# Performance work log

Measured on AMD Instinct MI355X. Metric: run time of the kernel, lower is better.

Reference implementation:

```python
import jax, jax.numpy as jnp
import numpy as np

# CycleFC1w1a constants (from init_kwargs / gen_offset)
IN_CH = 384
KH, KW = 1, 7  # cycle kernel; actual conv weight is 1x1
START = (KH * KW) // 2  # 3


def _gen_offset_x(C):
    # kernel_size[0] == 1 branch: off_y = 0, off_x[i] = (i + START) % KW - KW // 2
    i = jnp.arange(C)
    return (i + START) % KW - KW // 2  # int32, values in [-3, 3]


def setup_inputs() -> dict:
    key = jax.random.key(0)
    k1, k2, k3 = jax.random.split(key, 3)
    x = jax.random.normal(k1, (64, IN_CH, 32, 32), dtype=jnp.float32)
    weight = jax.random.normal(k2, (IN_CH, IN_CH), dtype=jnp.float32) * 0.05  # [out_ch, in_ch]
    bias = jax.random.normal(k3, (IN_CH,), dtype=jnp.float32) * 0.01
    return {"x": x, "weight": weight, "bias": bias}


def reference(x, weight, bias):
    B, C, H, W = x.shape
    # BinaryQuantizer forward: sign()
    xb = jnp.sign(x)
    wb = jnp.sign(weight)  # [O, C]

    # Fixed per-channel integer horizontal offsets -> exact shifted gather
    off_x = _gen_offset_x(C)                                  # [C]
    cols = jnp.arange(W)[None, :] + off_x[:, None]            # [C, W] sample col = w + off
    valid = (cols >= 0) & (cols < W)                          # zero-pad out of bounds
    cols_c = jnp.clip(cols, 0, W - 1)
    # gather along width per channel: [B, C, H, W]
    g = jnp.take_along_axis(xb, cols_c[None, :, None, :], axis=3)
    g = g * valid[None, :, None, :].astype(x.dtype)

    # pointwise (1x1) channel-mixing conv
    out = jnp.einsum('bchw,oc->bohw', g, wb) + bias[None, :, None, None]
    return out
```

## Files before the change

### kernel.cpp

```cpp
#include <hip/hip_runtime.h>
#include <stdint.h>


#define IN_CH 384
#define HH 32
#define WW 32
#define BB 64

constexpr uint64_t P7(int t) {
  uint64_t m = 0;
  for (int k = 0; k < 64; ++k)
    if (k % 7 == t) m |= (1ull << k);
  return m;
}
__device__ __constant__ uint64_t Pm[7] = {P7(0), P7(1), P7(2), P7(3), P7(4), P7(5), P7(6)};

__global__ __launch_bounds__(64) void cyc_prep(const float* __restrict__ wgt,
                                               const float* __restrict__ bias,
                                               uint64_t* __restrict__ wbg,
                                               float* __restrict__ bias2w) {
  const int o = blockIdx.x;
  const int lane = threadIdx.x;
  __shared__ uint64_t wb_sh[6];
#pragma unroll
  for (int j = 0; j < 6; ++j) {
    uint64_t m = __ballot(wgt[o * IN_CH + j * 64 + lane] < 0.0f);
    if (lane == 0) wb_sh[j] = m;
  }
  __syncthreads();
  if (lane < 6) wbg[o * 6 + lane] = wb_sh[lane];
  if (lane < WW) {
    const int w = lane;
    int nv = 0, corr = 0;
#pragma unroll
    for (int j = 0; j < 6; ++j) {
      uint64_t V = 0;
#pragma unroll
      for (int d = -3; d <= 3; ++d) {
        int wd = w + d;
        if (wd >= 0 && wd < WW) V |= Pm[(d - j + 14) % 7];
      }
      nv += __popcll(V);
      corr += __popcll(wb_sh[j] & ~V);
    }
    bias2w[o * WW + w] = bias[o] + (float)nv + 2.0f * (float)corr;
  }
}

__global__ __launch_bounds__(768) void cyc_pack(const float* __restrict__ x,
                                                uint32_t* __restrict__ G32) {
  const int t = threadIdx.x;
  const int lane = t & 63, wave = t >> 6;
  const int b = blockIdx.x >> 3;
  const int h0 = (blockIdx.x & 7) * 4;
  const int wcol = lane & 31, hhalf = lane >> 5;
#pragma unroll
  for (int p = 0; p < 2; ++p) {
    const int tau = wave + p * 12;
    const int r = tau / 6, j = tau % 6;
    const int c = j * 64 + lane;
    const int off = ((c % 7 + 3) % 7) - 3;
    const uint32_t shr = (off > 0) ? (uint32_t)off : 0u;
    const uint32_t shl = (off < 0) ? (uint32_t)(-off) : 0u;
    const float4* xp = reinterpret_cast<const float4*>(
        x + (size_t)((b * IN_CH + c) * HH + h0 + r) * WW);
    uint32_t myw = 0;
#pragma unroll
    for (int i = 0; i < 8; ++i) {
      float4 v = xp[i];
      myw |= (v.x < 0.0f ? 1u : 0u) << (i * 4 + 0);
      myw |= (v.y < 0.0f ? 1u : 0u) << (i * 4 + 1);
      myw |= (v.z < 0.0f ? 1u : 0u) << (i * 4 + 2);
      myw |= (v.w < 0.0f ? 1u : 0u) << (i * 4 + 3);
    }
    uint32_t s = (myw >> shr) << shl;
    constexpr uint32_t Mt[5] = {0xFFFF0000u, 0xFF00FF00u, 0xF0F0F0F0u,
                                0xCCCCCCCCu, 0xAAAAAAAAu};
#pragma unroll
    for (int stp = 0; stp < 5; ++stp) {
      const int js = 16 >> stp;
      const uint32_t M = Mt[stp];
      uint32_t y = __shfl_xor(s, js);
      s = (lane & js) ? ((s & M) | ((y >> js) & ~M))
                      : ((s & ~M) | ((y << js) & M));
    }
    G32[(((size_t)b * 6 + j) * 1024 + (h0 + r) * 32 + wcol) * 2 + hhalf] = s;
  }
}

__global__ __launch_bounds__(512) void cyc_gemm(const uint64_t* __restrict__ G,
                                                const uint64_t* __restrict__ wbg,
                                                const float* __restrict__ bias2w,
                                                float* __restrict__ out) {
  const int t = threadIdx.x;
  const int lane = t & 63, wave = t >> 6;
  const int b = blockIdx.x >> 3;
  const int oc = blockIdx.x & 7;
  const int o0 = oc * 48 + __builtin_amdgcn_readfirstlane(wave) * 6;

  uint64_t Wg[6][6];
  {
    const uint64_t* wp = wbg + (size_t)o0 * 6;
#pragma unroll
    for (int oo = 0; oo < 6; ++oo)
#pragma unroll
      for (int j = 0; j < 6; ++j) Wg[oo][j] = wp[oo * 6 + j];
  }
  const int w4 = (4 * lane) & 31;
  float4 bs[6];
#pragma unroll
  for (int oo = 0; oo < 6; ++oo)
    bs[oo] = *reinterpret_cast<const float4*>(bias2w + (o0 + oo) * WW + w4);

  const uint64_t* gb = G + (size_t)b * 6 * 1024;
  float* ob = out + ((size_t)b * IN_CH + o0) * (HH * WW);

#pragma unroll
  for (int pass = 0; pass < 4; ++pass) {
    const int p0 = pass * 256 + 4 * lane;
    uint64_t ga[6], gB[6], gc[6], gd[6];
#pragma unroll
    for (int j = 0; j < 6; ++j) {
      const ulonglong2* gp =
          reinterpret_cast<const ulonglong2*>(gb + (size_t)j * 1024 + p0);
      ulonglong2 u = gp[0], v = gp[1];
      ga[j] = u.x; gB[j] = u.y; gc[j] = v.x; gd[j] = v.y;
    }
#pragma unroll
    for (int oo = 0; oo < 6; ++oo) {
      int m0 = 0, m1 = 0, m2 = 0, m3 = 0;
#pragma unroll
      for (int j = 0; j < 6; ++j) {
        m0 += __popcll(ga[j] ^ Wg[oo][j]);
        m1 += __popcll(gB[j] ^ Wg[oo][j]);
        m2 += __popcll(gc[j] ^ Wg[oo][j]);
        m3 += __popcll(gd[j] ^ Wg[oo][j]);
      }
      float4 r;
      r.x = bs[oo].x - 2.0f * (float)m0;
      r.y = bs[oo].y - 2.0f * (float)m1;
      r.z = bs[oo].z - 2.0f * (float)m2;
      r.w = bs[oo].w - 2.0f * (float)m3;
      *reinterpret_cast<float4*>(ob + (size_t)oo * (HH * WW) + p0) = r;
    }
  }
}

extern "C" void kernel_launch(void* const* d_in, const int* in_sizes, int n_in,
                              void* d_out, int out_size, void* d_ws, size_t ws_size,
                              hipStream_t stream) {
  const float* x = (const float*)d_in[0];
  const float* wgt = (const float*)d_in[1];
  const float* bias = (const float*)d_in[2];
  float* out = (float*)d_out;

  uint64_t* wbg = (uint64_t*)d_ws;
  float* bias2w = (float*)((char*)d_ws + 18432);
  uint64_t* G = (uint64_t*)((char*)d_ws + 67584);

  cyc_prep<<<IN_CH, 64, 0, stream>>>(wgt, bias, wbg, bias2w);
  cyc_pack<<<BB * 8, 768, 0, stream>>>(x, (uint32_t*)G);
  cyc_gemm<<<BB * 8, 512, 0, stream>>>(G, wbg, bias2w, out);
}
```

Before: 197.5 us.

## Regrid pack and gemm kernels into smaller blocks with more loads in flight

The pack kernel now uses 384-thread blocks, one wave per 64-channel group. Each thread loads two full rows (h and h+16) up front before packing, so more memory requests are outstanding at once. The gemm kernel is split into 2048 blocks of 256 threads, each covering 24 output channels and half the spatial positions, with every lane handling 2 positions instead of 4. The aim is higher occupancy and better latency hiding for this bandwidth-bound work, at the cost of narrower float2 stores and more blocks that each reload the weights.

Result: slower. 378.4 us (+91.6%).

```diff
diff --git a/kernel.cpp b/kernel.cpp
--- a/kernel.cpp
+++ b/kernel.cpp
@@ -47,56 +47,79 @@
   }
 }
 
-__global__ __launch_bounds__(768) void cyc_pack(const float* __restrict__ x,
-                                                uint32_t* __restrict__ G32) {
+__device__ __forceinline__ uint32_t pack_row(const float4* __restrict__ xp,
+                                             float4 (&v)[8]) {
+  uint32_t myw = 0;
+#pragma unroll
+  for (int i = 0; i < 8; ++i) {
+    myw |= (v[i].x < 0.0f ? 1u : 0u) << (i * 4 + 0);
+    myw |= (v[i].y < 0.0f ? 1u : 0u) << (i * 4 + 1);
+    myw |= (v[i].z < 0.0f ? 1u : 0u) << (i * 4 + 2);
+    myw |= (v[i].w < 0.0f ? 1u : 0u) << (i * 4 + 3);
+  }
+  return myw;
+}
+
+__device__ __forceinline__ uint32_t bfly32(uint32_t s, int lane) {
+  constexpr uint32_t Mt[5] = {0xFFFF0000u, 0xFF00FF00u, 0xF0F0F0F0u,
+                              0xCCCCCCCCu, 0xAAAAAAAAu};
+#pragma unroll
+  for (int stp = 0; stp < 5; ++stp) {
+    const int js = 16 >> stp;
+    const uint32_t M = Mt[stp];
+    uint32_t y = __shfl_xor(s, js);
+    s = (lane & js) ? ((s & M) | ((y >> js) & ~M))
+                    : ((s & ~M) | ((y << js) & M));
+  }
+  return s;
+}
+
+__global__ __launch_bounds__(384, 6) void cyc_pack(const float* __restrict__ x,
+                                                   uint32_t* __restrict__ G32) {
+  const int t = threadIdx.x;
+  const int lane = t & 63, j = t >> 6;
+  const int b = blockIdx.x >> 4;
+  const int h = blockIdx.x & 15;
+  const int wcol = lane & 31, hhalf = lane >> 5;
+
+  const int c = j * 64 + lane;
+  const int off = ((c % 7 + 3) % 7) - 3;
+  const uint32_t shr = (off > 0) ? (uint32_t)off : 0u;
+  const uint32_t shl = (off < 0) ? (uint32_t)(-off) : 0u;
+
+  const float* xc = x + (size_t)(b * IN_CH + c) * (HH * WW);
+  const float4* xpa = reinterpret_cast<const float4*>(xc + h * WW);
+  const float4* xpb = reinterpret_cast<const float4*>(xc + (h + 16) * WW);
+
+  float4 va[8], vb[8];
+#pragma unroll
+  for (int i = 0; i < 8; ++i) va[i] = xpa[i];
+#pragma unroll
+  for (int i = 0; i < 8; ++i) vb[i] = xpb[i];
+
+  uint32_t sa = pack_row(xpa, va);
+  uint32_t sb = pack_row(xpb, vb);
+  sa = (sa >> shr) << shl;
+  sb = (sb >> shr) << shl;
+  sa = bfly32(sa, lane);
+  sb = bfly32(sb, lane);
+
+  uint32_t* gout = G32 + ((size_t)b * 6 + j) * 2048;
+  gout[((h)*32 + wcol) * 2 + hhalf] = sa;
+  gout[((h + 16) * 32 + wcol) * 2 + hhalf] = sb;
+}
+
+__global__ __launch_bounds__(256, 8) void cyc_gemm(const uint64_t* __restrict__ G,
+                                                   const uint64_t* __restrict__ wbg,
+                                                   const float* __restrict__ bias2w,
+                                                   float* __restrict__ out) {
   const int t = threadIdx.x;
   const int lane = t & 63, wave = t >> 6;
-  const int b = blockIdx.x >> 3;
-  const int h0 = (blockIdx.x & 7) * 4;
-  const int wcol = lane & 31, hhalf = lane >> 5;
-#pragma unroll
-  for (int p = 0; p < 2; ++p) {
-    const int tau = wave + p * 12;
-    const int r = tau / 6, j = tau % 6;
-    const int c = j * 64 + lane;
-    const int off = ((c % 7 + 3) % 7) - 3;
-    const uint32_t shr = (off > 0) ? (uint32_t)off : 0u;
-    const uint32_t shl = (off < 0) ? (uint32_t)(-off) : 0u;
-    const float4* xp = reinterpret_cast<const float4*>(
-        x + (size_t)((b * IN_CH + c) * HH + h0 + r) * WW);
-    uint32_t myw = 0;
-#pragma unroll
-    for (int i = 0; i < 8; ++i) {
-      float4 v = xp[i];
-      myw |= (v.x < 0.0f ? 1u : 0u) << (i * 4 + 0);
-      myw |= (v.y < 0.0f ? 1u : 0u) << (i * 4 + 1);
-      myw |= (v.z < 0.0f ? 1u : 0u) << (i * 4 + 2);
-      myw |= (v.w < 0.0f ? 1u : 0u) << (i * 4 + 3);
-    }
-    uint32_t s = (myw >> shr) << shl;
-    constexpr uint32_t Mt[5] = {0xFFFF0000u, 0xFF00FF00u, 0xF0F0F0F0u,
-                                0xCCCCCCCCu, 0xAAAAAAAAu};
-#pragma unroll
-    for (int stp = 0; stp < 5; ++stp) {
-      const int js = 16 >> stp;
-      const uint32_t M = Mt[stp];
-      uint32_t y = __shfl_xor(s, js);
-      s = (lane & js) ? ((s & M) | ((y >> js) & ~M))
-                      : ((s & ~M) | ((y << js) & M));
-    }
-    G32[(((size_t)b * 6 + j) * 1024 + (h0 + r) * 32 + wcol) * 2 + hhalf] = s;
-  }
-}
-
-__global__ __launch_bounds__(512) void cyc_gemm(const uint64_t* __restrict__ G,
-                                                const uint64_t* __restrict__ wbg,
-                                                const float* __restrict__ bias2w,
-                                                float* __restrict__ out) {
-  const int t = threadIdx.x;
-  const int lane = t & 63, wave = t >> 6;
-  const int b = blockIdx.x >> 3;
-  const int oc = blockIdx.x & 7;
-  const int o0 = oc * 48 + __builtin_amdgcn_readfirstlane(wave) * 6;
+  const int bid = blockIdx.x;
+  const int ph = bid & 1;
+  const int oc = (bid >> 1) & 15;
+  const int b = bid >> 5;
+  const int o0 = oc * 24 + __builtin_amdgcn_readfirstlane(wave) * 6;
 
   uint64_t Wg[6][6];
   {
@@ -106,42 +129,38 @@
 #pragma unroll
       for (int j = 0; j < 6; ++j) Wg[oo][j] = wp[oo * 6 + j];
   }
-  const int w4 = (4 * lane) & 31;
-  float4 bs[6];
+  const int w2 = (2 * lane) & 31;
+  float2 bs[6];
 #pragma unroll
   for (int oo = 0; oo < 6; ++oo)
-    bs[oo] = *reinterpret_cast<const float4*>(bias2w + (o0 + oo) * WW + w4);
+    bs[oo] = *reinterpret_cast<const float2*>(bias2w + (o0 + oo) * WW + w2);
 
   const uint64_t* gb = G + (size_t)b * 6 * 1024;
   float* ob = out + ((size_t)b * IN_CH + o0) * (HH * WW);
 
 #pragma unroll
   for (int pass = 0; pass < 4; ++pass) {
-    const int p0 = pass * 256 + 4 * lane;
-    uint64_t ga[6], gB[6], gc[6], gd[6];
+    const int p0 = ph * 512 + pass * 128 + 2 * lane;
+    uint64_t ga[6], gc[6];
 #pragma unroll
     for (int j = 0; j < 6; ++j) {
-      const ulonglong2* gp =
-          reinterpret_cast<const ulonglong2*>(gb + (size_t)j * 1024 + p0);
-      ulonglong2 u = gp[0], v = gp[1];
-      ga[j] = u.x; gB[j] = u.y; gc[j] = v.x; gd[j] = v.y;
+      const ulonglong2 u =
+          *reinterpret_cast<const ulonglong2*>(gb + (size_t)j * 1024 + p0);
+      ga[j] = u.x;
+      gc[j] = u.y;
     }
 #pragma unroll
     for (int oo = 0; oo < 6; ++oo) {
-      int m0 = 0, m1 = 0, m2 = 0, m3 = 0;
+      int m0 = 0, m1 = 0;
 #pragma unroll
       for (int j = 0; j < 6; ++j) {
         m0 += __popcll(ga[j] ^ Wg[oo][j]);
-        m1 += __popcll(gB[j] ^ Wg[oo][j]);
-        m2 += __popcll(gc[j] ^ Wg[oo][j]);
-        m3 += __popcll(gd[j] ^ Wg[oo][j]);
+        m1 += __popcll(gc[j] ^ Wg[oo][j]);
       }
-      float4 r;
+      float2 r;
       r.x = bs[oo].x - 2.0f * (float)m0;
       r.y = bs[oo].y - 2.0f * (float)m1;
-      r.z = bs[oo].z - 2.0f * (float)m2;
-      r.w = bs[oo].w - 2.0f * (float)m3;
-      *reinterpret_cast<float4*>(ob + (size_t)oo * (HH * WW) + p0) = r;
+      *reinterpret_cast<float2*>(ob + (size_t)oo * (HH * WW) + p0) = r;
     }
   }
 }
@@ -159,6 +178,6 @@
   uint64_t* G = (uint64_t*)((char*)d_ws + 67584);
 
   cyc_prep<<<IN_CH, 64, 0, stream>>>(wgt, bias, wbg, bias2w);
-  cyc_pack<<<BB * 8, 768, 0, stream>>>(x, (uint32_t*)G);
-  cyc_gemm<<<BB * 8, 512, 0, stream>>>(G, wbg, bias2w, out);
+  cyc_pack<<<BB * 16, 384, 0, stream>>>(x, (uint32_t*)G);
+  cyc_gemm<<<BB * 16 * 2, 256, 0, stream>>>(G, wbg, bias2w, out);
 }
```
